# Performance work log

Hardware: AMD Instinct MI355X
Metric: run time of the kernel (lower is better)

The kernel has to match this reference:

```python
import jax, jax.numpy as jnp
import numpy as np

DIM = 64
B_GRAPHS = 16
N_NODES = 4096
N_EDGES = 16384
SLOPE = 0.01  # PyTorch leaky_relu default negative slope


def lrelu(x):
    return jnp.where(x >= 0, x, SLOPE * x)


def setup_inputs() -> dict:
    key = jax.random.key(0)
    ks = jax.random.split(key, 16)
    d = DIM

    def rn(k, shape, scale=0.05):
        return jax.random.normal(k, shape, dtype=jnp.float32) * scale

    def z(*s):
        return jnp.zeros(s, jnp.float32)

    return {
        "x": jax.random.normal(ks[0], (N_NODES, 3), dtype=jnp.float32),
        "edge_attr": jax.random.normal(ks[1], (N_EDGES, 4), dtype=jnp.float32),
        "edge_index": jax.random.randint(ks[2], (2, N_EDGES), 0, N_NODES),
        "batch": jnp.sort(jax.random.randint(ks[3], (N_NODES,), 0, B_GRAPHS)),
        # lin0
        "W0": rn(ks[4], (3, d)), "b0": z(d),
        # edge MLP: Linear(4,d) -> LeakyReLU -> Linear(d, d*d)
        "We1": rn(ks[5], (4, d)), "be1": z(d),
        "We2": rn(ks[6], (d, d * d), 0.01), "be2": z(d * d),
        # NNConv root weight + bias
        "root": rn(ks[7], (d, d)), "conv_b": z(d),
        # GRU(d, d)  (PyTorch layout: [3d, in] / [3d, hid], gate order r,z,n)
        "Wih": rn(ks[8], (3 * d, d)), "Whh": rn(ks[9], (3 * d, d)),
        "bih": z(3 * d), "bhh": z(3 * d),
        # Set2Set LSTM(2d, d)  (gate order i,f,g,o)
        "lWih": rn(ks[10], (4 * d, 2 * d)), "lWhh": rn(ks[11], (4 * d, d)),
        "lbih": z(4 * d), "lbhh": z(4 * d),
        # lin_out: Linear(2d, 2)
        "Wout": rn(ks[12], (2 * d, 2)), "bout": z(2),
    }


def _forward(x, edge_attr, W0, b0, We1, be1, We2, be2, root, conv_b,
             Wih, Whh, bih, bhh, lWih, lWhh, lbih, lbhh, Wout, bout,
             edge_index, batch):
    d = DIM
    N = x.shape[0]
    E = edge_attr.shape[0]
    src, dst = edge_index[0], edge_index[1]  # messages flow src(j) -> dst(i)

    out = lrelu(x @ W0 + b0)  # [N, d]
    h = out                    # GRU hidden state (h = out.unsqueeze(0))

    # Edge-conditioned weights: constant across the 6 iterations, compute once.
    he = lrelu(edge_attr @ We1 + be1)          # [E, d]
    W_e = (he @ We2 + be2).reshape(E, d, d)    # [E, d, d]
    deg = jax.ops.segment_sum(jnp.ones((E,), jnp.float32), dst, num_segments=N)
    inv_deg = (1.0 / jnp.maximum(deg, 1.0))[:, None]  # mean aggr, clamp like PyG

    for _ in range(6):
        # NNConv: gather x_j, per-edge matmul, scatter-mean, plus root term
        msg = jnp.einsum('ed,edf->ef', out[src], W_e)            # [E, d]
        agg = jax.ops.segment_sum(msg, dst, num_segments=N) * inv_deg
        m = lrelu(agg + out @ root + conv_b)                     # [N, d]
        # GRU cell (single step, PyTorch gate order r, z, n)
        gi = m @ Wih.T + bih
        gh = h @ Whh.T + bhh
        i_r, i_z, i_n = jnp.split(gi, 3, axis=-1)
        h_r, h_z, h_n = jnp.split(gh, 3, axis=-1)
        r = jax.nn.sigmoid(i_r + h_r)
        zg = jax.nn.sigmoid(i_z + h_z)
        n = jnp.tanh(i_n + r * h_n)
        h = (1.0 - zg) * n + zg * h
        out = h

    # Set2Set pooling, processing_steps = 1
    Bg = B_GRAPHS
    q_star = jnp.zeros((Bg, 2 * d), jnp.float32)
    hl = jnp.zeros((Bg, d), jnp.float32)
    cl = jnp.zeros((Bg, d), jnp.float32)
    gates = q_star @ lWih.T + lbih + hl @ lWhh.T + lbhh
    gi_, gf_, gg_, go_ = jnp.split(gates, 4, axis=-1)
    cl = jax.nn.sigmoid(gf_) * cl + jax.nn.sigmoid(gi_) * jnp.tanh(gg_)
    q = jax.nn.sigmoid(go_) * jnp.tanh(cl)         # [Bg, d]
    e = jnp.sum(out * q[batch], axis=-1)           # [N]
    emax = jax.ops.segment_max(e, batch, num_segments=Bg)
    a = jnp.exp(e - emax[batch])
    asum = jax.ops.segment_sum(a, batch, num_segments=Bg)
    a = a / asum[batch]                            # per-graph softmax attention
    rpool = jax.ops.segment_sum(a[:, None] * out, batch, num_segments=Bg)
    q_star = jnp.concatenate([q, rpool], axis=-1)  # [Bg, 2d]

    return q_star @ Wout + bout                    # [Bg, 2]


def reference(x, edge_attr, edge_index, batch, W0, b0, We1, be1, We2, be2,
              root, conv_b, Wih, Whh, bih, bhh, lWih, lWhh, lbih, lbhh,
              Wout, bout):
    return _forward(x, edge_attr, W0, b0, We1, be1, We2, be2, root, conv_b,
                    Wih, Whh, bih, bhh, lWih, lWhh, lbih, lbhh, Wout, bout,
                    edge_index, batch)
```

## Files before the change

### kernel.cpp

```cpp
#include <hip/hip_runtime.h>
#include <cstddef>

#define NE 16384
#define NN 4096
#define BG 16
#define CSTR 4416

__device__ __forceinline__ float lrelu(float v){ return v >= 0.f ? v : 0.01f*v; }
__device__ __forceinline__ float sigm(float v){ return 1.f/(1.f + expf(-v)); }

__global__ __launch_bounds__(256) void setup_kernel(
    const float* __restrict__ x, const float* __restrict__ ea,
    const int* __restrict__ ei,
    const float* __restrict__ W0, const float* __restrict__ b0,
    const float* __restrict__ We1, const float* __restrict__ be1,
    const float* __restrict__ We2, const float* __restrict__ be2,
    const float* __restrict__ root, const float* __restrict__ Whh,
    const float* __restrict__ Wih,
    float* __restrict__ Baug, float* __restrict__ WihT,
    float* __restrict__ h, float* __restrict__ he,
    int* __restrict__ deg, int* __restrict__ cnt)
{
    int t = blockIdx.x*256 + threadIdx.x;
    {
        int e = t >> 6, f = t & 63;
        float v = be1[f];
        #pragma unroll
        for (int d = 0; d < 4; ++d) v += ea[e*4+d]*We1[d*64+f];
        he[t] = lrelu(v);
    }
    if (t < 64*CSTR) {
        int d = t / CSTR, c = t - d*CSTR;
        float v;
        if (c < 4096)      v = We2[(c>>6)*4096 + d*64 + (c&63)];
        else if (c < 4160) v = be2[d*64 + (c-4096)];
        else if (c < 4352) v = Whh[(c-4160)*64 + d];
        else               v = root[d*64 + (c-4352)];
        Baug[t] = v;
    }
    if (t < NN*64) {
        int n = t >> 6, f = t & 63;
        float v = b0[f];
        #pragma unroll
        for (int d = 0; d < 3; ++d) v += x[n*3+d]*W0[d*64+f];
        h[t] = lrelu(v);
    }
    if (t < 12288) { int k = t / 192; WihT[t] = Wih[(t - k*192)*64 + k]; }
    if (t < NE) {
        atomicAdd(&deg[ei[NE + t]], 1);
        atomicAdd(&cnt[ei[t]], 1);
    }
}

__global__ __launch_bounds__(256) void scan_kernel(const int* __restrict__ cnt,
                                                   int* __restrict__ offs)
{
    __shared__ int ps[256];
    int t = threadIdx.x;
    int base = t*16;
    int loc[16];
    int s = 0;
    #pragma unroll
    for (int i = 0; i < 16; ++i) { loc[i] = s; s += cnt[base+i]; }
    ps[t] = s; __syncthreads();
    for (int off = 1; off < 256; off <<= 1) {
        int v = 0;
        if (t >= off) v = ps[t-off];
        __syncthreads();
        if (t >= off) ps[t] += v;
        __syncthreads();
    }
    int pre = (t == 0) ? 0 : ps[t-1];
    #pragma unroll
    for (int i = 0; i < 16; ++i) offs[base+i] = pre + loc[i];
    if (t == 255) offs[NN] = pre + s;
}

__global__ __launch_bounds__(256) void scatter_kernel(
    const int* __restrict__ ei, const int* __restrict__ offs,
    int* __restrict__ cnt,
    int* __restrict__ srcs, int* __restrict__ dsts, int* __restrict__ perm)
{
    int e = blockIdx.x*256 + threadIdx.x;
    if (e >= NE) return;
    int s = ei[e], d = ei[NE + e];
    int old = atomicSub(&cnt[s], 1);
    int pos = offs[s] + old - 1;
    srcs[pos] = s; dsts[pos] = d; perm[pos] = e;
}

__global__ __launch_bounds__(256) void inv_range_kernel(
    const int* __restrict__ deg, const int* __restrict__ batch,
    float* __restrict__ inv_deg, int* __restrict__ gstart, int* __restrict__ gend)
{
    int n = blockIdx.x*256 + threadIdx.x;
    if (n >= NN) return;
    inv_deg[n] = 1.f / fmaxf((float)deg[n], 1.f);
    int b  = batch[n];
    int bp = (n == 0)    ? -1 : batch[n-1];
    int bn = (n == NN-1) ? BG : batch[n+1];
    for (int g = bp+1; g <= b; ++g) gstart[g] = n;
    for (int g = b;   g <  bn; ++g) gend[g]   = n+1;
    if (n == 0)    for (int g = 0;   g < b;  ++g) gend[g]   = 0;
    if (n == NN-1) for (int g = b+1; g < BG; ++g) gstart[g] = NN;
}

__global__ __launch_bounds__(256) void gemm_big(
    const float* __restrict__ h, const float* __restrict__ Baug,
    float* __restrict__ C, float* __restrict__ agg)
{
    __shared__ float As[64][132];
    int t = threadIdx.x;
    int bx = blockIdx.x;
    int by = blockIdx.y;
    int m0 = by*128, c0 = bx*128;

    if (bx == 0) {
        float* a = agg + by*8192;
        #pragma unroll
        for (int i = 0; i < 32; ++i) a[t + i*256] = 0.f;
    }
    #pragma unroll
    for (int i = 0; i < 8; ++i) {
        int idx4 = t + i*256;
        int r = idx4 >> 4;
        int kc = (idx4 & 15) * 4;
        const float4 v = *(const float4*)(h + (size_t)(m0 + r)*64 + kc);
        As[kc+0][r] = v.x; As[kc+1][r] = v.y; As[kc+2][r] = v.z; As[kc+3][r] = v.w;
    }
    __syncthreads();

    int tx = t & 15, ty = t >> 4;
    int c_lo = c0 + tx*4, c_hi = c0 + 64 + tx*4;
    bool hi_ok = (c0 + 64) < CSTR;

    float acc[8][8];
    #pragma unroll
    for (int i = 0; i < 8; ++i)
        #pragma unroll
        for (int j = 0; j < 8; ++j) acc[i][j] = 0.f;

    #pragma unroll 8
    for (int k = 0; k < 64; ++k) {
        float4 a0 = *(const float4*)&As[k][ty*4];
        float4 a1 = *(const float4*)&As[k][64 + ty*4];
        float4 b0 = *(const float4*)(Baug + (size_t)k*CSTR + c_lo);
        float4 b1 = hi_ok ? *(const float4*)(Baug + (size_t)k*CSTR + c_hi)
                          : make_float4(0.f,0.f,0.f,0.f);
        float av[8] = {a0.x,a0.y,a0.z,a0.w,a1.x,a1.y,a1.z,a1.w};
        float bv[8] = {b0.x,b0.y,b0.z,b0.w,b1.x,b1.y,b1.z,b1.w};
        #pragma unroll
        for (int i = 0; i < 8; ++i)
            #pragma unroll
            for (int j = 0; j < 8; ++j) acc[i][j] += av[i]*bv[j];
    }

    #pragma unroll
    for (int i = 0; i < 8; ++i) {
        int m = m0 + (i>>2)*64 + ty*4 + (i&3);
        float* Cr = C + (size_t)m*CSTR;
        *(float4*)(Cr + c_lo) = make_float4(acc[i][0],acc[i][1],acc[i][2],acc[i][3]);
        if (hi_ok)
            *(float4*)(Cr + c_hi) = make_float4(acc[i][4],acc[i][5],acc[i][6],acc[i][7]);
    }
}

__global__ __launch_bounds__(256) void edge_kernel(
    const float* __restrict__ C, const float* __restrict__ he,
    const int* __restrict__ srcs, const int* __restrict__ dsts,
    const int* __restrict__ perm, float* __restrict__ agg)
{
    __shared__ float hs[256];
    int t = threadIdx.x;
    int e0 = blockIdx.x*4;
    int w = t >> 6, f = t & 63;
    int es = e0 + w;
    int pe = perm[es];
    hs[t] = he[(size_t)pe*64 + f];
    int src = srcs[es], dst = dsts[es];
    __syncthreads();
    const float* Cs = C + (size_t)src*CSTR;
    float m = Cs[4096 + f];
    #pragma unroll 8
    for (int k = 0; k < 64; ++k) m += hs[w*64+k] * Cs[k*64 + f];
    atomicAdd(&agg[(size_t)dst*64 + f], m);
}

__global__ __launch_bounds__(256) void node_kernel(
    const float* __restrict__ C, const float* __restrict__ agg,
    const float* __restrict__ inv_deg, const float* __restrict__ conv_b,
    const float* __restrict__ WihT, const float* __restrict__ bih,
    const float* __restrict__ bhh, float* __restrict__ h)
{
    __shared__ float WT[64][196];
    __shared__ float mT[64][18];
    int t = threadIdx.x;
    int n0 = blockIdx.x * 16;
    #pragma unroll
    for (int i = 0; i < 48; ++i) {
        int idx = t + i*256;
        int k = idx / 192;
        WT[k][idx - k*192] = WihT[idx];
    }
    #pragma unroll
    for (int i = 0; i < 4; ++i) {
        int idx = t + i*256;
        int n = idx >> 6, d = idx & 63;
        int gn = n0 + n;
        float v = agg[(size_t)gn*64 + d]*inv_deg[gn]
                + C[(size_t)gn*CSTR + 4352 + d] + conv_b[d];
        mT[d][n] = lrelu(v);
    }
    __syncthreads();

    int tx = t & 31, ty = t >> 5;
    float acc[2][2][3] = {};
    for (int k = 0; k < 64; ++k) {
        float2 a  = *(float2*)&mT[k][ty*2];
        float2 br = *(float2*)&WT[k][tx*2];
        float2 bz = *(float2*)&WT[k][64 + tx*2];
        float2 bn = *(float2*)&WT[k][128 + tx*2];
        acc[0][0][0] += a.x*br.x; acc[0][1][0] += a.x*br.y;
        acc[1][0][0] += a.y*br.x; acc[1][1][0] += a.y*br.y;
        acc[0][0][1] += a.x*bz.x; acc[0][1][1] += a.x*bz.y;
        acc[1][0][1] += a.y*bz.x; acc[1][1][1] += a.y*bz.y;
        acc[0][0][2] += a.x*bn.x; acc[0][1][2] += a.x*bn.y;
        acc[1][0][2] += a.y*bn.x; acc[1][1][2] += a.y*bn.y;
    }
    #pragma unroll
    for (int i = 0; i < 2; ++i) {
        int n = n0 + ty*2 + i;
        const float* Cn = C + (size_t)n*CSTR;
        #pragma unroll
        for (int j = 0; j < 2; ++j) {
            int g = tx*2 + j;
            float ir  = acc[i][j][0] + bih[g];
            float iz  = acc[i][j][1] + bih[64+g];
            float in_ = acc[i][j][2] + bih[128+g];
            float r  = sigm(ir  + Cn[4160 + g]       + bhh[g]);
            float z  = sigm(iz  + Cn[4160 + 64 + g]  + bhh[64+g]);
            float nn = tanhf(in_ + r*(Cn[4160 + 128 + g] + bhh[128+g]));
            float ho = h[(size_t)n*64 + g];
            h[(size_t)n*64 + g] = (1.f - z)*nn + z*ho;
        }
    }
}

__device__ __forceinline__ float q_val(const float* lbih, const float* lbhh, int g)
{
    float gi = lbih[g]     + lbhh[g];
    float gg = lbih[128+g] + lbhh[128+g];
    float go = lbih[192+g] + lbhh[192+g];
    return sigm(go)*tanhf(sigm(gi)*tanhf(gg));
}

__global__ __launch_bounds__(256) void e_kernel(
    const float* __restrict__ h, const float* __restrict__ lbih,
    const float* __restrict__ lbhh, float* __restrict__ e)
{
    __shared__ float qs[64];
    int t = threadIdx.x;
    if (t < 64) qs[t] = q_val(lbih, lbhh, t);
    __syncthreads();
    int w = t >> 6, f = t & 63;
    int n = blockIdx.x*4 + w;
    float p = h[(size_t)n*64 + f]*qs[f];
    #pragma unroll
    for (int off = 32; off; off >>= 1) p += __shfl_xor(p, off);
    if (f == 0) e[n] = p;
}

__global__ __launch_bounds__(1024) void pool_kernel(
    const float* __restrict__ h, float* __restrict__ e,
    const int* __restrict__ gstart, const int* __restrict__ gend,
    const float* __restrict__ lbih, const float* __restrict__ lbhh,
    const float* __restrict__ Wout, const float* __restrict__ bout,
    float* __restrict__ out)
{
    __shared__ float red[1024];
    __shared__ float rp[64];
    __shared__ float sval;
    int g = blockIdx.x, t = threadIdx.x;
    int s = gstart[g], en = gend[g];

    float mx = -1e30f;
    for (int n = s+t; n < en; n += 1024) mx = fmaxf(mx, e[n]);
    red[t] = mx; __syncthreads();
    for (int st = 512; st; st >>= 1) { if (t < st) red[t] = fmaxf(red[t], red[t+st]); __syncthreads(); }
    if (t == 0) sval = red[0];
    __syncthreads();
    float lmx = sval;
    __syncthreads();

    float sm = 0.f;
    for (int n = s+t; n < en; n += 1024) { float a = expf(e[n]-lmx); e[n] = a; sm += a; }
    red[t] = sm; __syncthreads();
    for (int st = 512; st; st >>= 1) { if (t < st) red[t] += red[t+st]; __syncthreads(); }
    if (t == 0) sval = (red[0] > 0.f) ? 1.f/red[0] : 0.f;
    __syncthreads();
    float inv_asum = sval;
    __syncthreads();

    int w = t >> 6, f = t & 63;
    float racc = 0.f;
    for (int n = s+w; n < en; n += 16) racc += e[n]*h[(size_t)n*64 + f];
    red[t] = racc; __syncthreads();
    if (w == 0) {
        float a = 0.f;
        #pragma unroll
        for (int i = 0; i < 16; ++i) a += red[i*64 + f];
        rp[f] = a*inv_asum;
    }
    __syncthreads();

    if (t < 64) {
        float qv = q_val(lbih, lbhh, t);
        float p0 = qv*Wout[t*2]   + rp[t]*Wout[(64+t)*2];
        float p1 = qv*Wout[t*2+1] + rp[t]*Wout[(64+t)*2+1];
        #pragma unroll
        for (int off = 32; off; off >>= 1) { p0 += __shfl_xor(p0, off); p1 += __shfl_xor(p1, off); }
        if (t == 0) { out[g*2] = p0 + bout[0]; out[g*2+1] = p1 + bout[1]; }
    }
}

extern "C" void kernel_launch(void* const* d_in, const int* in_sizes, int n_in,
                              void* d_out, int out_size, void* d_ws, size_t ws_size,
                              hipStream_t stream)
{
    const float* x      = (const float*)d_in[0];
    const float* ea     = (const float*)d_in[1];
    const int*   ei     = (const int*)  d_in[2];
    const int*   batch  = (const int*)  d_in[3];
    const float* W0     = (const float*)d_in[4];
    const float* b0     = (const float*)d_in[5];
    const float* We1    = (const float*)d_in[6];
    const float* be1    = (const float*)d_in[7];
    const float* We2    = (const float*)d_in[8];
    const float* be2    = (const float*)d_in[9];
    const float* root   = (const float*)d_in[10];
    const float* conv_b = (const float*)d_in[11];
    const float* Wih    = (const float*)d_in[12];
    const float* Whh    = (const float*)d_in[13];
    const float* bih    = (const float*)d_in[14];
    const float* bhh    = (const float*)d_in[15];
    const float* lbih   = (const float*)d_in[18];
    const float* lbhh   = (const float*)d_in[19];
    const float* Wout   = (const float*)d_in[20];
    const float* bout   = (const float*)d_in[21];
    float* out = (float*)d_out;

    float* W = (float*)d_ws;
    size_t off = 0;
    float* C       = W + off; off += (size_t)NN*CSTR;
    float* Baug    = W + off; off += (size_t)64*CSTR;
    float* h       = W + off; off += (size_t)NN*64;
    float* he      = W + off; off += (size_t)NE*64;
    float* agg     = W + off; off += (size_t)NN*64;
    float* WihT    = W + off; off += 12288;
    float* inv_deg = W + off; off += NN;
    float* e       = W + off; off += NN;
    int*   deg     = (int*)(W + off); off += NN;
    int*   cnt     = (int*)(W + off); off += NN;
    int*   offs    = (int*)(W + off); off += NN+1;
    int*   srcs    = (int*)(W + off); off += NE;
    int*   dsts    = (int*)(W + off); off += NE;
    int*   perm    = (int*)(W + off); off += NE;
    int*   gstart  = (int*)(W + off); off += BG;
    int*   gend    = (int*)(W + off); off += BG;

    hipMemsetAsync(deg, 0, 2*NN*sizeof(int), stream);
    setup_kernel<<<4096, 256, 0, stream>>>(x, ea, ei, W0, b0, We1, be1, We2, be2,
                                           root, Whh, Wih, Baug, WihT, h, he, deg, cnt);
    scan_kernel<<<1, 256, 0, stream>>>(cnt, offs);
    scatter_kernel<<<64, 256, 0, stream>>>(ei, offs, cnt, srcs, dsts, perm);
    inv_range_kernel<<<16, 256, 0, stream>>>(deg, batch, inv_deg, gstart, gend);

    for (int it = 0; it < 6; ++it) {
        gemm_big<<<dim3(35, 32), 256, 0, stream>>>(h, Baug, C, agg);
        edge_kernel<<<NE/4, 256, 0, stream>>>(C, he, srcs, dsts, perm, agg);
        node_kernel<<<NN/16, 256, 0, stream>>>(C, agg, inv_deg, conv_b, WihT, bih, bhh, h);
    }

    e_kernel<<<NN/4, 256, 0, stream>>>(h, lbih, lbhh, e);
    pool_kernel<<<BG, 1024, 0, stream>>>(h, e, gstart, gend, lbih, lbhh, Wout, bout, out);
}
```

Baseline: 657.1 us.

## Fuse per-node We2 projection with edge aggregation, drop the large C buffer

Replaces the big GEMM that wrote a 4096x4416 intermediate C and the separate edge kernel with a fused kernel. The fused kernel computes each source node's h·We2 projection in registers using readlane broadcasts, then contracts it with the edge features of that node's outgoing edges and atomically adds the result into agg. The root and Whh products move into node_kernel as small per-node dot products, and node_kernel now zeroes agg after reading it. This removes the roughly 72 MB per-iteration write and read of C. The trade-offs are serial per-node edge loops with block-wide syncs, uneven edge counts per node, and heavy register use (64 accumulators plus 16 h values per thread).

```diff
diff --git a/kernel.cpp b/kernel.cpp
--- a/kernel.cpp
+++ b/kernel.cpp
@@ -4,22 +4,22 @@
 #define NE 16384
 #define NN 4096
 #define BG 16
-#define CSTR 4416
 
 __device__ __forceinline__ float lrelu(float v){ return v >= 0.f ? v : 0.01f*v; }
 __device__ __forceinline__ float sigm(float v){ return 1.f/(1.f + expf(-v)); }
+__device__ __forceinline__ float rl(float v, int l){
+    return __int_as_float(__builtin_amdgcn_readlane(__float_as_int(v), l));
+}
 
 __global__ __launch_bounds__(256) void setup_kernel(
     const float* __restrict__ x, const float* __restrict__ ea,
     const int* __restrict__ ei,
     const float* __restrict__ W0, const float* __restrict__ b0,
     const float* __restrict__ We1, const float* __restrict__ be1,
-    const float* __restrict__ We2, const float* __restrict__ be2,
-    const float* __restrict__ root, const float* __restrict__ Whh,
-    const float* __restrict__ Wih,
-    float* __restrict__ Baug, float* __restrict__ WihT,
+    const float* __restrict__ Whh, const float* __restrict__ Wih,
+    float* __restrict__ WihT, float* __restrict__ WhhT,
     float* __restrict__ h, float* __restrict__ he,
-    int* __restrict__ deg, int* __restrict__ cnt)
+    int* __restrict__ deg, int* __restrict__ cnt, float* __restrict__ agg)
 {
     int t = blockIdx.x*256 + threadIdx.x;
     {
@@ -29,23 +29,19 @@
         for (int d = 0; d < 4; ++d) v += ea[e*4+d]*We1[d*64+f];
         he[t] = lrelu(v);
     }
-    if (t < 64*CSTR) {
-        int d = t / CSTR, c = t - d*CSTR;
-        float v;
-        if (c < 4096)      v = We2[(c>>6)*4096 + d*64 + (c&63)];
-        else if (c < 4160) v = be2[d*64 + (c-4096)];
-        else if (c < 4352) v = Whh[(c-4160)*64 + d];
-        else               v = root[d*64 + (c-4352)];
-        Baug[t] = v;
-    }
     if (t < NN*64) {
         int n = t >> 6, f = t & 63;
         float v = b0[f];
         #pragma unroll
         for (int d = 0; d < 3; ++d) v += x[n*3+d]*W0[d*64+f];
         h[t] = lrelu(v);
-    }
-    if (t < 12288) { int k = t / 192; WihT[t] = Wih[(t - k*192)*64 + k]; }
+        agg[t] = 0.f;
+    }
+    if (t < 12288) {
+        int k = t / 192, g = t - k*192;
+        WihT[t] = Wih[g*64 + k];
+        WhhT[t] = Whh[g*64 + k];
+    }
     if (t < NE) {
         atomicAdd(&deg[ei[NE + t]], 1);
         atomicAdd(&cnt[ei[t]], 1);
@@ -79,14 +75,14 @@
 __global__ __launch_bounds__(256) void scatter_kernel(
     const int* __restrict__ ei, const int* __restrict__ offs,
     int* __restrict__ cnt,
-    int* __restrict__ srcs, int* __restrict__ dsts, int* __restrict__ perm)
+    int* __restrict__ dsts, int* __restrict__ perm)
 {
     int e = blockIdx.x*256 + threadIdx.x;
     if (e >= NE) return;
     int s = ei[e], d = ei[NE + e];
     int old = atomicSub(&cnt[s], 1);
     int pos = offs[s] + old - 1;
-    srcs[pos] = s; dsts[pos] = d; perm[pos] = e;
+    dsts[pos] = d; perm[pos] = e;
 }
 
 __global__ __launch_bounds__(256) void inv_range_kernel(
@@ -105,95 +101,94 @@
     if (n == NN-1) for (int g = b+1; g < BG; ++g) gstart[g] = NN;
 }
 
-__global__ __launch_bounds__(256) void gemm_big(
-    const float* __restrict__ h, const float* __restrict__ Baug,
-    float* __restrict__ C, float* __restrict__ agg)
-{
-    __shared__ float As[64][132];
+__global__ __launch_bounds__(512) void fused_msg(
+    const float* __restrict__ h, const float* __restrict__ We2,
+    const float* __restrict__ be2, const float* __restrict__ he,
+    const int* __restrict__ offs, const int* __restrict__ dsts,
+    const int* __restrict__ perm, float* __restrict__ agg)
+{
+    __shared__ float tmp[8][4][64];
+    __shared__ float bias[16][64];
     int t = threadIdx.x;
-    int bx = blockIdx.x;
-    int by = blockIdx.y;
-    int m0 = by*128, c0 = bx*128;
-
-    if (bx == 0) {
-        float* a = agg + by*8192;
-        #pragma unroll
-        for (int i = 0; i < 32; ++i) a[t + i*256] = 0.f;
-    }
-    #pragma unroll
-    for (int i = 0; i < 8; ++i) {
-        int idx4 = t + i*256;
-        int r = idx4 >> 4;
-        int kc = (idx4 & 15) * 4;
-        const float4 v = *(const float4*)(h + (size_t)(m0 + r)*64 + kc);
-        As[kc+0][r] = v.x; As[kc+1][r] = v.y; As[kc+2][r] = v.z; As[kc+3][r] = v.w;
-    }
-    __syncthreads();
-
-    int tx = t & 15, ty = t >> 4;
-    int c_lo = c0 + tx*4, c_hi = c0 + 64 + tx*4;
-    bool hi_ok = (c0 + 64) < CSTR;
-
-    float acc[8][8];
-    #pragma unroll
-    for (int i = 0; i < 8; ++i)
-        #pragma unroll
-        for (int j = 0; j < 8; ++j) acc[i][j] = 0.f;
-
-    #pragma unroll 8
-    for (int k = 0; k < 64; ++k) {
-        float4 a0 = *(const float4*)&As[k][ty*4];
-        float4 a1 = *(const float4*)&As[k][64 + ty*4];
-        float4 b0 = *(const float4*)(Baug + (size_t)k*CSTR + c_lo);
-        float4 b1 = hi_ok ? *(const float4*)(Baug + (size_t)k*CSTR + c_hi)
-                          : make_float4(0.f,0.f,0.f,0.f);
-        float av[8] = {a0.x,a0.y,a0.z,a0.w,a1.x,a1.y,a1.z,a1.w};
-        float bv[8] = {b0.x,b0.y,b0.z,b0.w,b1.x,b1.y,b1.z,b1.w};
-        #pragma unroll
-        for (int i = 0; i < 8; ++i)
-            #pragma unroll
-            for (int j = 0; j < 8; ++j) acc[i][j] += av[i]*bv[j];
-    }
-
-    #pragma unroll
-    for (int i = 0; i < 8; ++i) {
-        int m = m0 + (i>>2)*64 + ty*4 + (i&3);
-        float* Cr = C + (size_t)m*CSTR;
-        *(float4*)(Cr + c_lo) = make_float4(acc[i][0],acc[i][1],acc[i][2],acc[i][3]);
-        if (hi_ok)
-            *(float4*)(Cr + c_hi) = make_float4(acc[i][4],acc[i][5],acc[i][6],acc[i][7]);
-    }
-}
-
-__global__ __launch_bounds__(256) void edge_kernel(
-    const float* __restrict__ C, const float* __restrict__ he,
-    const int* __restrict__ srcs, const int* __restrict__ dsts,
-    const int* __restrict__ perm, float* __restrict__ agg)
-{
-    __shared__ float hs[256];
-    int t = threadIdx.x;
-    int e0 = blockIdx.x*4;
-    int w = t >> 6, f = t & 63;
-    int es = e0 + w;
-    int pe = perm[es];
-    hs[t] = he[(size_t)pe*64 + f];
-    int src = srcs[es], dst = dsts[es];
-    __syncthreads();
-    const float* Cs = C + (size_t)src*CSTR;
-    float m = Cs[4096 + f];
-    #pragma unroll 8
-    for (int k = 0; k < 64; ++k) m += hs[w*64+k] * Cs[k*64 + f];
-    atomicAdd(&agg[(size_t)dst*64 + f], m);
+    int lane = t & 63, w = t >> 6;
+    int n0 = blockIdx.x * 16;
+    int k0 = blockIdx.y * 32;
+    int kb = k0 + w*4;
+
+    float h_reg[16];
+    #pragma unroll
+    for (int n = 0; n < 16; ++n) h_reg[n] = h[(size_t)(n0+n)*64 + lane];
+
+    if (blockIdx.y == 0) {
+        #pragma unroll
+        for (int p = 0; p < 2; ++p) {
+            int idx = t + p*512;
+            int n = idx >> 6;
+            float acc_b = 0.f;
+            for (int d = 0; d < 64; ++d)
+                acc_b += rl(h_reg[n], d) * be2[d*64 + lane];
+            bias[n][lane] = acc_b;
+        }
+    }
+
+    float acc[4][16];
+    #pragma unroll
+    for (int j = 0; j < 4; ++j)
+        #pragma unroll
+        for (int n = 0; n < 16; ++n) acc[j][n] = 0.f;
+
+    const float* wp = We2 + (size_t)kb*4096 + lane;
+    #pragma unroll 4
+    for (int d = 0; d < 64; ++d) {
+        float a0 = wp[d*64];
+        float a1 = wp[4096  + d*64];
+        float a2 = wp[8192  + d*64];
+        float a3 = wp[12288 + d*64];
+        #pragma unroll
+        for (int n = 0; n < 16; ++n) {
+            float hv = rl(h_reg[n], d);
+            acc[0][n] += hv*a0; acc[1][n] += hv*a1;
+            acc[2][n] += hv*a2; acc[3][n] += hv*a3;
+        }
+    }
+    __syncthreads();
+
+    #pragma unroll
+    for (int n = 0; n < 16; ++n) {
+        int a = offs[n0+n], b = offs[n0+n+1];
+        for (int eb = a; eb < b; eb += 4) {
+            int cnt4 = min(4, b-eb);
+            for (int j2 = 0; j2 < cnt4; ++j2) {
+                int pe = perm[eb+j2];
+                const float* hep = he + (size_t)pe*64 + kb;
+                float part = hep[0]*acc[0][n] + hep[1]*acc[1][n]
+                           + hep[2]*acc[2][n] + hep[3]*acc[3][n];
+                tmp[w][j2][lane] = part;
+            }
+            __syncthreads();
+            if (w < cnt4) {
+                int e = eb + w;
+                float s = tmp[0][w][lane];
+                #pragma unroll
+                for (int ww = 1; ww < 8; ++ww) s += tmp[ww][w][lane];
+                if (blockIdx.y == 0) s += bias[n][lane];
+                atomicAdd(&agg[(size_t)dsts[e]*64 + lane], s);
+            }
+            __syncthreads();
+        }
+    }
 }
 
 __global__ __launch_bounds__(256) void node_kernel(
-    const float* __restrict__ C, const float* __restrict__ agg,
-    const float* __restrict__ inv_deg, const float* __restrict__ conv_b,
-    const float* __restrict__ WihT, const float* __restrict__ bih,
-    const float* __restrict__ bhh, float* __restrict__ h)
+    float* __restrict__ agg, const float* __restrict__ inv_deg,
+    const float* __restrict__ conv_b, const float* __restrict__ root,
+    const float* __restrict__ WhhT, const float* __restrict__ WihT,
+    const float* __restrict__ bih, const float* __restrict__ bhh,
+    float* __restrict__ h)
 {
     __shared__ float WT[64][196];
     __shared__ float mT[64][18];
+    __shared__ float h_lds[16][64];
     int t = threadIdx.x;
     int n0 = blockIdx.x * 16;
     #pragma unroll
@@ -205,11 +200,20 @@
     #pragma unroll
     for (int i = 0; i < 4; ++i) {
         int idx = t + i*256;
-        int n = idx >> 6, d = idx & 63;
+        h_lds[idx>>6][idx&63] = h[(size_t)n0*64 + idx];
+    }
+    __syncthreads();
+
+    #pragma unroll
+    for (int i = 0; i < 4; ++i) {
+        int idx = t + i*256;
+        int n = idx >> 6, dd = idx & 63;
         int gn = n0 + n;
-        float v = agg[(size_t)gn*64 + d]*inv_deg[gn]
-                + C[(size_t)gn*CSTR + 4352 + d] + conv_b[d];
-        mT[d][n] = lrelu(v);
+        float mr = 0.f;
+        for (int d = 0; d < 64; ++d) mr += h_lds[n][d]*root[d*64 + dd];
+        float av = agg[(size_t)gn*64 + dd];
+        agg[(size_t)gn*64 + dd] = 0.f;
+        mT[dd][n] = lrelu(av*inv_deg[gn] + mr + conv_b[dd]);
     }
     __syncthreads();
 
@@ -227,21 +231,26 @@
         acc[0][0][2] += a.x*bn.x; acc[0][1][2] += a.x*bn.y;
         acc[1][0][2] += a.y*bn.x; acc[1][1][2] += a.y*bn.y;
     }
-    #pragma unroll
-    for (int i = 0; i < 2; ++i) {
-        int n = n0 + ty*2 + i;
-        const float* Cn = C + (size_t)n*CSTR;
-        #pragma unroll
-        for (int j = 0; j < 2; ++j) {
-            int g = tx*2 + j;
-            float ir  = acc[i][j][0] + bih[g];
-            float iz  = acc[i][j][1] + bih[64+g];
-            float in_ = acc[i][j][2] + bih[128+g];
-            float r  = sigm(ir  + Cn[4160 + g]       + bhh[g]);
-            float z  = sigm(iz  + Cn[4160 + 64 + g]  + bhh[64+g]);
-            float nn = tanhf(in_ + r*(Cn[4160 + 128 + g] + bhh[128+g]));
-            float ho = h[(size_t)n*64 + g];
-            h[(size_t)n*64 + g] = (1.f - z)*nn + z*ho;
+
+    #pragma unroll
+    for (int j = 0; j < 2; ++j) {
+        int g = tx*2 + j;
+        #pragma unroll
+        for (int i = 0; i < 2; ++i) {
+            int n  = ty*2 + i;
+            int gn = n0 + n;
+            float ghr = bhh[g], ghz = bhh[64+g], ghn = bhh[128+g];
+            for (int d = 0; d < 64; ++d) {
+                float hv = h_lds[n][d];
+                ghr += hv*WhhT[d*192 + g];
+                ghz += hv*WhhT[d*192 + 64 + g];
+                ghn += hv*WhhT[d*192 + 128 + g];
+            }
+            float r  = sigm(acc[i][j][0] + bih[g]      + ghr);
+            float z  = sigm(acc[i][j][1] + bih[64+g]   + ghz);
+            float nn = tanhf(acc[i][j][2] + bih[128+g] + r*ghn);
+            float ho = h_lds[n][g];
+            h[(size_t)gn*64 + g] = (1.f - z)*nn + z*ho;
         }
     }
 }
@@ -351,34 +360,32 @@
 
     float* W = (float*)d_ws;
     size_t off = 0;
-    float* C       = W + off; off += (size_t)NN*CSTR;
-    float* Baug    = W + off; off += (size_t)64*CSTR;
     float* h       = W + off; off += (size_t)NN*64;
     float* he      = W + off; off += (size_t)NE*64;
     float* agg     = W + off; off += (size_t)NN*64;
     float* WihT    = W + off; off += 12288;
+    float* WhhT    = W + off; off += 12288;
     float* inv_deg = W + off; off += NN;
     float* e       = W + off; off += NN;
     int*   deg     = (int*)(W + off); off += NN;
     int*   cnt     = (int*)(W + off); off += NN;
     int*   offs    = (int*)(W + off); off += NN+1;
-    int*   srcs    = (int*)(W + off); off += NE;
     int*   dsts    = (int*)(W + off); off += NE;
     int*   perm    = (int*)(W + off); off += NE;
     int*   gstart  = (int*)(W + off); off += BG;
     int*   gend    = (int*)(W + off); off += BG;
 
     hipMemsetAsync(deg, 0, 2*NN*sizeof(int), stream);
-    setup_kernel<<<4096, 256, 0, stream>>>(x, ea, ei, W0, b0, We1, be1, We2, be2,
-                                           root, Whh, Wih, Baug, WihT, h, he, deg, cnt);
+    setup_kernel<<<4096, 256, 0, stream>>>(x, ea, ei, W0, b0, We1, be1,
+                                           Whh, Wih, WihT, WhhT, h, he, deg, cnt, agg);
     scan_kernel<<<1, 256, 0, stream>>>(cnt, offs);
-    scatter_kernel<<<64, 256, 0, stream>>>(ei, offs, cnt, srcs, dsts, perm);
+    scatter_kernel<<<64, 256, 0, stream>>>(ei, offs, cnt, dsts, perm);
     inv_range_kernel<<<16, 256, 0, stream>>>(deg, batch, inv_deg, gstart, gend);
 
     for (int it = 0; it < 6; ++it) {
-        gemm_big<<<dim3(35, 32), 256, 0, stream>>>(h, Baug, C, agg);
-        edge_kernel<<<NE/4, 256, 0, stream>>>(C, he, srcs, dsts, perm, agg);
-        node_kernel<<<NN/16, 256, 0, stream>>>(C, agg, inv_deg, conv_b, WihT, bih, bhh, h);
+        fused_msg<<<dim3(NN/16, 2), 512, 0, stream>>>(h, We2, be2, he, offs, dsts, perm, agg);
+        node_kernel<<<NN/16, 256, 0, stream>>>(agg, inv_deg, conv_b, root, WhhT,
+                                               WihT, bih, bhh, h);
     }
 
     e_kernel<<<NN/4, 256, 0, stream>>>(h, lbih, lbhh, e);
```

After: 1.364 ms. 2.08x slower.

## Fuse per-node edge-weight GEMM with CSR edge message aggregation in shared memory

Applied to the files above, without the earlier changes.

The large per-node GEMM (h times the reshaped We2, about 4096x4416 floats written to global memory and then re-read by the edge kernel) is replaced by a fused kernel. Each block computes a 128-node by 128-column tile, keeps it in shared memory, and immediately reduces the src-sorted edges whose source nodes lie in that tile, accumulating into agg with atomics. The small bias, Whh and root products move into a separate 320-column GEMM. The fused kernel also adds XOR swizzling for its shared-memory tile, a one-time permuted copy of he, and zeroing of agg inside node_kernel. This removes roughly 72 MB of global write and read traffic per iteration, at the cost of an extra small kernel and warp-shuffle reductions in the edge loop.

```diff
diff --git a/kernel.cpp b/kernel.cpp
--- a/kernel.cpp
+++ b/kernel.cpp
@@ -4,7 +4,6 @@
 #define NE 16384
 #define NN 4096
 #define BG 16
-#define CSTR 4416
 
 __device__ __forceinline__ float lrelu(float v){ return v >= 0.f ? v : 0.01f*v; }
 __device__ __forceinline__ float sigm(float v){ return 1.f/(1.f + expf(-v)); }
@@ -17,9 +16,9 @@
     const float* __restrict__ We2, const float* __restrict__ be2,
     const float* __restrict__ root, const float* __restrict__ Whh,
     const float* __restrict__ Wih,
-    float* __restrict__ Baug, float* __restrict__ WihT,
+    float* __restrict__ Bp, float* __restrict__ BsmT, float* __restrict__ WihT,
     float* __restrict__ h, float* __restrict__ he,
-    int* __restrict__ deg, int* __restrict__ cnt)
+    int* __restrict__ deg, int* __restrict__ cnt, float* __restrict__ agg)
 {
     int t = blockIdx.x*256 + threadIdx.x;
     {
@@ -29,21 +28,26 @@
         for (int d = 0; d < 4; ++d) v += ea[e*4+d]*We1[d*64+f];
         he[t] = lrelu(v);
     }
-    if (t < 64*CSTR) {
-        int d = t / CSTR, c = t - d*CSTR;
-        float v;
-        if (c < 4096)      v = We2[(c>>6)*4096 + d*64 + (c&63)];
-        else if (c < 4160) v = be2[d*64 + (c-4096)];
-        else if (c < 4352) v = Whh[(c-4160)*64 + d];
-        else               v = root[d*64 + (c-4352)];
-        Baug[t] = v;
-    }
     if (t < NN*64) {
         int n = t >> 6, f = t & 63;
         float v = b0[f];
         #pragma unroll
         for (int d = 0; d < 3; ++d) v += x[n*3+d]*W0[d*64+f];
         h[t] = lrelu(v);
+        agg[t] = 0.f;
+    }
+    if (t < 64*4096) {
+        int d = t >> 12, r = t & 4095;
+        int f = r >> 6, k = r & 63;
+        Bp[t] = We2[(size_t)k*4096 + d*64 + f];
+    }
+    if (t < 320*64) {
+        int c = t >> 6, d = t & 63;
+        float v;
+        if (c < 64)       v = be2[d*64 + c];
+        else if (c < 256) v = Whh[(c-64)*64 + d];
+        else              v = root[d*64 + (c-256)];
+        BsmT[t] = v;
     }
     if (t < 12288) { int k = t / 192; WihT[t] = Wih[(t - k*192)*64 + k]; }
     if (t < NE) {
@@ -87,6 +91,15 @@
     int old = atomicSub(&cnt[s], 1);
     int pos = offs[s] + old - 1;
     srcs[pos] = s; dsts[pos] = d; perm[pos] = e;
+}
+
+__global__ __launch_bounds__(256) void heperm_kernel(
+    const float* __restrict__ he, const int* __restrict__ perm,
+    float* __restrict__ he_s)
+{
+    int t = blockIdx.x*256 + threadIdx.x;
+    int pos = t >> 6, f = t & 63;
+    he_s[t] = he[(size_t)perm[pos]*64 + f];
 }
 
 __global__ __launch_bounds__(256) void inv_range_kernel(
@@ -105,89 +118,125 @@
     if (n == NN-1) for (int g = b+1; g < BG; ++g) gstart[g] = NN;
 }
 
-__global__ __launch_bounds__(256) void gemm_big(
-    const float* __restrict__ h, const float* __restrict__ Baug,
-    float* __restrict__ C, float* __restrict__ agg)
-{
-    __shared__ float As[64][132];
+__global__ __launch_bounds__(256) void csm_gemm(
+    const float* __restrict__ h, const float* __restrict__ BsmT,
+    float* __restrict__ Csm)
+{
+    __shared__ float ht[16][64];
+    int t = threadIdx.x;
+    int n0 = blockIdx.x * 16;
+    #pragma unroll
+    for (int i = 0; i < 4; ++i) {
+        int idx = t + i*256;
+        ht[idx>>6][idx&63] = h[(size_t)n0*64 + idx];
+    }
+    __syncthreads();
+    for (int idx = t; idx < 16*320; idx += 256) {
+        int r = idx / 320, c = idx - r*320;
+        const float* bt = BsmT + (size_t)c*64;
+        const float* hr = ht[r];
+        float s = 0.f;
+        #pragma unroll 8
+        for (int d = 0; d < 64; d += 4) {
+            float4 a = *(const float4*)(hr + d);
+            float4 b = *(const float4*)(bt + d);
+            s += a.x*b.x + a.y*b.y + a.z*b.z + a.w*b.w;
+        }
+        Csm[(size_t)(n0+r)*320 + c] = s;
+    }
+}
+
+__global__ __launch_bounds__(256) void fused_msg(
+    const float* __restrict__ h, const float* __restrict__ Bp,
+    const float* __restrict__ he_s, const float* __restrict__ Csm,
+    const int* __restrict__ offs, const int* __restrict__ srcs,
+    const int* __restrict__ dsts, float* __restrict__ agg)
+{
+    __shared__ float buf[128*128];
     int t = threadIdx.x;
     int bx = blockIdx.x;
     int by = blockIdx.y;
     int m0 = by*128, c0 = bx*128;
 
-    if (bx == 0) {
-        float* a = agg + by*8192;
-        #pragma unroll
-        for (int i = 0; i < 32; ++i) a[t + i*256] = 0.f;
-    }
+    {
+        float (*As)[132] = (float(*)[132])buf;
+        #pragma unroll
+        for (int i = 0; i < 8; ++i) {
+            int idx4 = t + i*256;
+            int r  = idx4 >> 4;
+            int kc = (idx4 & 15) * 4;
+            float4 v = *(const float4*)(h + (size_t)(m0 + r)*64 + kc);
+            int cs = r ^ ((idx4 & 7) * 4);
+            As[kc+0][cs] = v.x; As[kc+1][cs] = v.y;
+            As[kc+2][cs] = v.z; As[kc+3][cs] = v.w;
+        }
+    }
+    __syncthreads();
+
+    int tx = t & 15, ty = t >> 4;
+    float acc[8][8];
+    #pragma unroll
+    for (int i = 0; i < 8; ++i)
+        #pragma unroll
+        for (int j = 0; j < 8; ++j) acc[i][j] = 0.f;
+
+    {
+        const float (*As)[132] = (const float(*)[132])buf;
+        #pragma unroll 8
+        for (int k = 0; k < 64; ++k) {
+            int sw = ((k >> 2) & 7) * 4;
+            float4 a0 = *(const float4*)&As[k][(ty*4) ^ sw];
+            float4 a1 = *(const float4*)&As[k][64 + ((ty*4) ^ sw)];
+            const float* bk = Bp + (size_t)k*4096 + c0 + tx*4;
+            float4 b0 = *(const float4*)bk;
+            float4 b1 = *(const float4*)(bk + 64);
+            float av[8] = {a0.x,a0.y,a0.z,a0.w,a1.x,a1.y,a1.z,a1.w};
+            float bv[8] = {b0.x,b0.y,b0.z,b0.w,b1.x,b1.y,b1.z,b1.w};
+            #pragma unroll
+            for (int i = 0; i < 8; ++i)
+                #pragma unroll
+                for (int j = 0; j < 8; ++j) acc[i][j] += av[i]*bv[j];
+        }
+    }
+    __syncthreads();
+
+    float (*G)[128] = (float(*)[128])buf;
     #pragma unroll
     for (int i = 0; i < 8; ++i) {
-        int idx4 = t + i*256;
-        int r = idx4 >> 4;
-        int kc = (idx4 & 15) * 4;
-        const float4 v = *(const float4*)(h + (size_t)(m0 + r)*64 + kc);
-        As[kc+0][r] = v.x; As[kc+1][r] = v.y; As[kc+2][r] = v.z; As[kc+3][r] = v.w;
-    }
-    __syncthreads();
-
-    int tx = t & 15, ty = t >> 4;
-    int c_lo = c0 + tx*4, c_hi = c0 + 64 + tx*4;
-    bool hi_ok = (c0 + 64) < CSTR;
-
-    float acc[8][8];
-    #pragma unroll
-    for (int i = 0; i < 8; ++i)
-        #pragma unroll
-        for (int j = 0; j < 8; ++j) acc[i][j] = 0.f;
-
-    #pragma unroll 8
-    for (int k = 0; k < 64; ++k) {
-        float4 a0 = *(const float4*)&As[k][ty*4];
-        float4 a1 = *(const float4*)&As[k][64 + ty*4];
-        float4 b0 = *(const float4*)(Baug + (size_t)k*CSTR + c_lo);
-        float4 b1 = hi_ok ? *(const float4*)(Baug + (size_t)k*CSTR + c_hi)
-                          : make_float4(0.f,0.f,0.f,0.f);
-        float av[8] = {a0.x,a0.y,a0.z,a0.w,a1.x,a1.y,a1.z,a1.w};
-        float bv[8] = {b0.x,b0.y,b0.z,b0.w,b1.x,b1.y,b1.z,b1.w};
-        #pragma unroll
-        for (int i = 0; i < 8; ++i)
-            #pragma unroll
-            for (int j = 0; j < 8; ++j) acc[i][j] += av[i]*bv[j];
-    }
-
-    #pragma unroll
-    for (int i = 0; i < 8; ++i) {
-        int m = m0 + (i>>2)*64 + ty*4 + (i&3);
-        float* Cr = C + (size_t)m*CSTR;
-        *(float4*)(Cr + c_lo) = make_float4(acc[i][0],acc[i][1],acc[i][2],acc[i][3]);
-        if (hi_ok)
-            *(float4*)(Cr + c_hi) = make_float4(acc[i][4],acc[i][5],acc[i][6],acc[i][7]);
-    }
-}
-
-__global__ __launch_bounds__(256) void edge_kernel(
-    const float* __restrict__ C, const float* __restrict__ he,
-    const int* __restrict__ srcs, const int* __restrict__ dsts,
-    const int* __restrict__ perm, float* __restrict__ agg)
-{
-    __shared__ float hs[256];
-    int t = threadIdx.x;
-    int e0 = blockIdx.x*4;
-    int w = t >> 6, f = t & 63;
-    int es = e0 + w;
-    int pe = perm[es];
-    hs[t] = he[(size_t)pe*64 + f];
-    int src = srcs[es], dst = dsts[es];
-    __syncthreads();
-    const float* Cs = C + (size_t)src*CSTR;
-    float m = Cs[4096 + f];
-    #pragma unroll 8
-    for (int k = 0; k < 64; ++k) m += hs[w*64+k] * Cs[k*64 + f];
-    atomicAdd(&agg[(size_t)dst*64 + f], m);
+        int m = (i>>2)*64 + ty*4 + (i&3);
+        *(float4*)&G[m][tx*4]      = make_float4(acc[i][0],acc[i][1],acc[i][2],acc[i][3]);
+        *(float4*)&G[m][64+tx*4]   = make_float4(acc[i][4],acc[i][5],acc[i][6],acc[i][7]);
+    }
+    __syncthreads();
+
+    int w = t >> 6, lane = t & 63;
+    int hf = lane >> 5, j = lane & 31;
+    int kk = j*2;
+    int est  = offs[m0];
+    int eend = offs[m0+128];
+    int f0 = bx*2;
+    for (int e = est + w*2 + hf; e < eend; e += 8) {
+        int src = srcs[e], dst = dsts[e];
+        int sl = src - m0;
+        float2 hv = *(const float2*)(he_s + (size_t)e*64 + kk);
+        float2 g0 = *(const float2*)&G[sl][kk];
+        float2 g1 = *(const float2*)&G[sl][64 + kk];
+        float p0 = hv.x*g0.x + hv.y*g0.y;
+        float p1 = hv.x*g1.x + hv.y*g1.y;
+        #pragma unroll
+        for (int o = 16; o >= 1; o >>= 1) {
+            p0 += __shfl_xor(p0, o);
+            p1 += __shfl_xor(p1, o);
+        }
+        if (j == 0) atomicAdd(&agg[(size_t)dst*64 + f0],
+                              p0 + Csm[(size_t)src*320 + f0]);
+        if (j == 1) atomicAdd(&agg[(size_t)dst*64 + f0 + 1],
+                              p1 + Csm[(size_t)src*320 + f0 + 1]);
+    }
 }
 
 __global__ __launch_bounds__(256) void node_kernel(
-    const float* __restrict__ C, const float* __restrict__ agg,
+    const float* __restrict__ Csm, float* __restrict__ agg,
     const float* __restrict__ inv_deg, const float* __restrict__ conv_b,
     const float* __restrict__ WihT, const float* __restrict__ bih,
     const float* __restrict__ bhh, float* __restrict__ h)
@@ -205,11 +254,12 @@
     #pragma unroll
     for (int i = 0; i < 4; ++i) {
         int idx = t + i*256;
-        int n = idx >> 6, d = idx & 63;
+        int n = idx >> 6, dd = idx & 63;
         int gn = n0 + n;
-        float v = agg[(size_t)gn*64 + d]*inv_deg[gn]
-                + C[(size_t)gn*CSTR + 4352 + d] + conv_b[d];
-        mT[d][n] = lrelu(v);
+        float av = agg[(size_t)gn*64 + dd];
+        agg[(size_t)gn*64 + dd] = 0.f;
+        float mr = Csm[(size_t)gn*320 + 256 + dd];
+        mT[dd][n] = lrelu(av*inv_deg[gn] + mr + conv_b[dd]);
     }
     __syncthreads();
 
@@ -230,16 +280,13 @@
     #pragma unroll
     for (int i = 0; i < 2; ++i) {
         int n = n0 + ty*2 + i;
-        const float* Cn = C + (size_t)n*CSTR;
+        const float* Cn = Csm + (size_t)n*320;
         #pragma unroll
         for (int j = 0; j < 2; ++j) {
             int g = tx*2 + j;
-            float ir  = acc[i][j][0] + bih[g];
-            float iz  = acc[i][j][1] + bih[64+g];
-            float in_ = acc[i][j][2] + bih[128+g];
-            float r  = sigm(ir  + Cn[4160 + g]       + bhh[g]);
-            float z  = sigm(iz  + Cn[4160 + 64 + g]  + bhh[64+g]);
-            float nn = tanhf(in_ + r*(Cn[4160 + 128 + g] + bhh[128+g]));
+            float r  = sigm(acc[i][j][0] + bih[g]     + Cn[64  + g] + bhh[g]);
+            float z  = sigm(acc[i][j][1] + bih[64+g]  + Cn[128 + g] + bhh[64+g]);
+            float nn = tanhf(acc[i][j][2] + bih[128+g] + r*(Cn[192 + g] + bhh[128+g]));
             float ho = h[(size_t)n*64 + g];
             h[(size_t)n*64 + g] = (1.f - z)*nn + z*ho;
         }
@@ -351,11 +398,13 @@
 
     float* W = (float*)d_ws;
     size_t off = 0;
-    float* C       = W + off; off += (size_t)NN*CSTR;
-    float* Baug    = W + off; off += (size_t)64*CSTR;
     float* h       = W + off; off += (size_t)NN*64;
     float* he      = W + off; off += (size_t)NE*64;
+    float* he_s    = W + off; off += (size_t)NE*64;
     float* agg     = W + off; off += (size_t)NN*64;
+    float* Bp      = W + off; off += (size_t)64*4096;
+    float* BsmT    = W + off; off += 320*64;
+    float* Csm     = W + off; off += (size_t)NN*320;
     float* WihT    = W + off; off += 12288;
     float* inv_deg = W + off; off += NN;
     float* e       = W + off; off += NN;
@@ -370,15 +419,19 @@
 
     hipMemsetAsync(deg, 0, 2*NN*sizeof(int), stream);
     setup_kernel<<<4096, 256, 0, stream>>>(x, ea, ei, W0, b0, We1, be1, We2, be2,
-                                           root, Whh, Wih, Baug, WihT, h, he, deg, cnt);
+                                           root, Whh, Wih, Bp, BsmT, WihT,
+                                           h, he, deg, cnt, agg);
     scan_kernel<<<1, 256, 0, stream>>>(cnt, offs);
     scatter_kernel<<<64, 256, 0, stream>>>(ei, offs, cnt, srcs, dsts, perm);
+    heperm_kernel<<<4096, 256, 0, stream>>>(he, perm, he_s);
     inv_range_kernel<<<16, 256, 0, stream>>>(deg, batch, inv_deg, gstart, gend);
 
     for (int it = 0; it < 6; ++it) {
-        gemm_big<<<dim3(35, 32), 256, 0, stream>>>(h, Baug, C, agg);
-        edge_kernel<<<NE/4, 256, 0, stream>>>(C, he, srcs, dsts, perm, agg);
-        node_kernel<<<NN/16, 256, 0, stream>>>(C, agg, inv_deg, conv_b, WihT, bih, bhh, h);
+        csm_gemm<<<NN/16, 256, 0, stream>>>(h, BsmT, Csm);
+        fused_msg<<<dim3(32, 32), 256, 0, stream>>>(h, Bp, he_s, Csm,
+                                                    offs, srcs, dsts, agg);
+        node_kernel<<<NN/16, 256, 0, stream>>>(Csm, agg, inv_deg, conv_b,
+                                               WihT, bih, bhh, h);
     }
 
     e_kernel<<<NN/4, 256, 0, stream>>>(h, lbih, lbhh, e);
```

New measurement: 1.639 ms. 2.49x slower.
